# Optimization experiments

Measured on AMD Instinct MI355X. Metric: run time of the kernel, lower is better.

## Reference

```python
import jax, jax.numpy as jnp
import numpy as np

VOCAB = 50257
WINDOW = 2048
EMB = 256
BATCH = 8


def setup_inputs() -> dict:
    key = jax.random.key(0)
    ks = jax.random.split(key, 9)
    s = 0.02
    x = jax.random.randint(ks[0], (BATCH, WINDOW), 0, VOCAB, dtype=jnp.int64 if jax.config.jax_enable_x64 else jnp.int32)
    tok_emb = jax.random.normal(ks[1], (VOCAB, EMB), dtype=jnp.float32) * s
    pos_emb = jax.random.normal(ks[2], (WINDOW, EMB), dtype=jnp.float32) * s
    Wq = jax.random.normal(ks[3], (EMB, EMB), dtype=jnp.float32) * s
    bq = jnp.zeros((EMB,), dtype=jnp.float32)
    Wk = jax.random.normal(ks[4], (EMB, EMB), dtype=jnp.float32) * s
    bk = jnp.zeros((EMB,), dtype=jnp.float32)
    Wv = jax.random.normal(ks[5], (EMB, EMB), dtype=jnp.float32) * s
    bv = jnp.zeros((EMB,), dtype=jnp.float32)
    return {"x": x, "tok_emb": tok_emb, "pos_emb": pos_emb,
            "Wq": Wq, "bq": bq, "Wk": Wk, "bk": bk, "Wv": Wv, "bv": bv}


def reference(x, tok_emb, pos_emb, Wq, bq, Wk, bk, Wv, bv):
    # h: [B, T, E] = token embedding + full-window position embedding
    h = tok_emb[x] + pos_emb[None, :, :]
    q = jnp.einsum('bte,fe->btf', h, Wq) + bq
    k = jnp.einsum('bte,fe->btf', h, Wk) + bk
    v = jnp.einsum('bte,fe->btf', h, Wv) + bv
    # NOTE: original module has NO 1/sqrt(d) scaling -- keep faithful.
    scores = jnp.einsum('bqe,bke->bqk', q, k)  # [B, T, T]
    T = scores.shape[-1]
    causal = jnp.tril(jnp.ones((T, T), dtype=bool))
    scores = jnp.where(causal[None, :, :], scores, -jnp.inf)
    weight = jax.nn.softmax(scores, axis=-1)
    attention_output = jnp.einsum('bqk,bke->bqe', weight, v)  # [B, T, E]
    return attention_output
```

## Files before the change

### kernel.cpp

```cpp
#include <hip/hip_runtime.h>


#define TWIN 2048
#define NEMB 256
#define NB   8
#define VOCAB 50257
#define NTOK (NB * TWIN)

typedef __attribute__((ext_vector_type(8))) short s16x8;
typedef __attribute__((ext_vector_type(4))) float f32x4;
typedef __attribute__((ext_vector_type(4))) float f4;
typedef unsigned short u16;
typedef unsigned int   u32;

__device__ __forceinline__ u16 f2bf(float f) {
    union { float f; u32 i; } x; x.f = f;
    u32 r = x.i + 0x7fffu + ((x.i >> 16) & 1u);
    return (u16)(r >> 16);
}
__device__ __forceinline__ float bf2f(u16 u) {
    union { u32 i; float f; } x; x.i = ((u32)u) << 16; return x.f;
}
__device__ __forceinline__ u32 pack2bf(float a, float b) {
    return (u32)f2bf(a) | ((u32)f2bf(b) << 16);
}
__device__ __forceinline__ void gload_lds16(const void* g, void* l) {
    __builtin_amdgcn_global_load_lds(
        (const __attribute__((address_space(1))) void*)g,
        (__attribute__((address_space(3))) void*)l, 16, 0, 0);
}

__global__ __launch_bounds__(256) void wconv_kernel(
    const float* __restrict__ Wq, const float* __restrict__ Wk,
    const float* __restrict__ Wv, u16* __restrict__ Wb)
{
    int b = blockIdx.x;
    int which = b >> 5;
    int off = (b & 31) * 2048 + threadIdx.x * 8;
    const float* src = (which == 0) ? Wq : ((which == 1) ? Wk : Wv);
    f4 v0 = *(const f4*)(src + off);
    f4 v1 = *(const f4*)(src + off + 4);
    u16 ww[8];
#pragma unroll
    for (int i = 0; i < 4; i++) { ww[i] = f2bf(v0[i]); ww[4 + i] = f2bf(v1[i]); }
    *(uint4*)(Wb + which * 65536 + off) = *(uint4*)ww;
}

__global__ __launch_bounds__(256) void tok_prep(const void* xraw, int* tokidx) {
    const long long* x64 = (const long long*)xraw;
    const int*       x32 = (const int*)xraw;
    long long probe = x64[threadIdx.x & 63];
    int ok = (probe >= 0 && probe < VOCAB) ? 1 : 0;
    int is64 = __all(ok);
    int i = blockIdx.x * 256 + threadIdx.x;
    int v = is64 ? (int)x64[i] : x32[i];
    tokidx[i] = (v < 0) ? 0 : ((v >= VOCAB) ? (VOCAB - 1) : v);
}

__global__ __launch_bounds__(128) void qkv_kernel(
    const int* __restrict__ tokidx,
    const float* __restrict__ tok, const float* __restrict__ pos,
    const u16* __restrict__ Wb,
    const float* __restrict__ bqp, const float* __restrict__ bkp,
    const float* __restrict__ bvp,
    u16* __restrict__ Qg, u16* __restrict__ Kg, u16* __restrict__ Vt)
{
    __shared__ u16 h_lds[32 * 256];

    const int tid   = threadIdx.x;
    const int which = blockIdx.x >> 9;
    const int t0    = (blockIdx.x & 511) * 32;
    const int bb    = t0 >> 11;
    const int tl0   = t0 & (TWIN - 1);

#pragma unroll
    for (int j = 0; j < 8; j++) {
        int c   = tid + 128 * j;
        int row = c >> 5, col = c & 31;
        int t   = t0 + row;
        int xi  = tokidx[t];
        const float* tp = tok + (size_t)xi * NEMB + col * 8;
        const float* pp = pos + (size_t)(t & (TWIN - 1)) * NEMB + col * 8;
        f4 a0 = *(const f4*)tp, a1 = *(const f4*)(tp + 4);
        f4 b0 = *(const f4*)pp, b1 = *(const f4*)(pp + 4);
        u16 hh[8];
#pragma unroll
        for (int i = 0; i < 4; i++) {
            hh[i]     = f2bf(a0[i] + b0[i]);
            hh[4 + i] = f2bf(a1[i] + b1[i]);
        }
        *(uint4*)((char*)h_lds + row * 512 + ((col * 16) ^ ((row & 7) << 4))) = *(uint4*)hh;
    }
    __syncthreads();

    const int wid = tid >> 6, lane = tid & 63, g = lane >> 4, lr = lane & 15;
    const u16* Wp = Wb + which * 65536;
    const float* Bp = (which == 0) ? bqp : ((which == 1) ? bkp : bvp);

    f32x4 acc[16];
#pragma unroll
    for (int i = 0; i < 16; i++) acc[i] = (f32x4){0.f, 0.f, 0.f, 0.f};

#pragma unroll
    for (int es = 0; es < 8; es++) {
        int arow = wid * 16 + lr;
        s16x8 af = *(const s16x8*)((const char*)h_lds + arow * 512 +
                                   ((es * 64 + g * 16) ^ ((arow & 7) << 4)));
        s16x8 bfv[16];
#pragma unroll
        for (int ct = 0; ct < 16; ct++)
            bfv[ct] = *(const s16x8*)(Wp + (size_t)(ct * 16 + lr) * NEMB + es * 32 + g * 8);
#pragma unroll
        for (int ct = 0; ct < 16; ct++)
            acc[ct] = __builtin_amdgcn_mfma_f32_16x16x32_bf16(af, bfv[ct], acc[ct], 0, 0, 0);
    }

    if (which < 2) {
        u16* dst = (which == 0) ? Qg : Kg;
        __syncthreads();
#pragma unroll
        for (int ct = 0; ct < 16; ct++) {
            float bias = Bp[ct * 16 + lr];
#pragma unroll
            for (int r = 0; r < 4; r++)
                h_lds[(wid * 16 + 4 * g + r) * 256 + ct * 16 + lr] = f2bf(acc[ct][r] + bias);
        }
        __syncthreads();
#pragma unroll
        for (int j = 0; j < 8; j++) {
            int c = tid + 128 * j;
            int row = c >> 5, col = c & 31;
            uint4 v = *(const uint4*)(h_lds + row * 256 + col * 8);
            *(uint4*)(dst + (size_t)(t0 + row) * NEMB + col * 8) = v;
        }
    } else {
#pragma unroll
        for (int ct = 0; ct < 16; ct++) {
            float bias = Bp[ct * 16 + lr];
            u16 pk[4];
#pragma unroll
            for (int r = 0; r < 4; r++) pk[r] = f2bf(acc[ct][r] + bias);
            int e = ct * 16 + lr;
            *(ushort4*)(Vt + ((size_t)bb * NEMB + e) * TWIN + tl0 + wid * 16 + 4 * g)
                = *(ushort4*)pk;
        }
    }
}

__global__ __launch_bounds__(256) void attn_partial(
    const u16* __restrict__ Qg, const u16* __restrict__ Kg,
    const u16* __restrict__ Vt, u16* __restrict__ Ppart,
    float* __restrict__ Pm, float* __restrict__ Pl)
{
    __shared__ char smem[65536];

    const int bid = blockIdx.x;
    const int bb  = bid & 7;
    const int idx = bid >> 3;
    int J, cc;
    if (idx < 17)      { J = 31 - idx; cc = 0; }
    else if (idx < 33) { J = 48 - idx; cc = 1; }
    else               { J = 47 - idx; cc = 0; }
    const int ntJ = 2 * J + 2;
    const int ts  = cc * 32;
    const int te  = (ntJ < ts + 32) ? ntJ : (ts + 32);
    const int n   = te - ts;
    const int cid = bb * 48 + ((cc == 0) ? J : (32 + J - 16));

    const u16* Qb = Qg + (size_t)bb * TWIN * NEMB;
    const u16* Kb = Kg + (size_t)bb * TWIN * NEMB;
    const u16* Vb = Vt + (size_t)bb * NEMB * TWIN;

    const int tid = threadIdx.x;
    const int w = tid >> 6, lane = tid & 63;
    const int q = lane & 15, hi = lane >> 4;
    const int qrow = J * 64 + w * 16 + q;

    s16x8 qf[8];
#pragma unroll
    for (int es = 0; es < 8; es++)
        qf[es] = *(const s16x8*)(Qb + (size_t)qrow * NEMB + es * 32 + hi * 8);

    #define STAGE(buf_, kb_)                                                          \
    {                                                                                 \
        char* base = smem + (buf_) * 32768;                                           \
        const int kbq_ = (kb_);                                                       \
        if (w < 2) {                                                                  \
            _Pragma("unroll")                                                         \
            for (int i2 = 0; i2 < 8; i2++) {                                          \
                int gc = w * 8 + i2;                                                  \
                int s = gc * 64 + lane;                                               \
                int row = s >> 5, col16 = s & 31;                                     \
                const char* src = (const char*)(Kb + (size_t)(kbq_ + row) * NEMB)     \
                                  + ((col16 * 16) ^ ((row & 7) << 4));                \
                gload_lds16(src, base + gc * 1024);                                   \
            }                                                                         \
        } else {                                                                      \
            _Pragma("unroll")                                                         \
            for (int i2 = 0; i2 < 8; i2++) {                                          \
                int gv = (w - 2) * 8 + i2;                                            \
                int s = gv * 64 + lane;                                               \
                int rr = s >> 8, ee = s & 255;                                        \
                const char* src = (const char*)(Vb + (size_t)ee * TWIN + kbq_ + rr * 8); \
                gload_lds16(src, base + 16384 + gv * 1024);                           \
            }                                                                         \
        }                                                                             \
    }

    STAGE(0, ts * 32)
    if (n > 1) STAGE(1, (ts + 1) * 32)

    f32x4 o[16];
#pragma unroll
    for (int i = 0; i < 16; i++) o[i] = (f32x4){0.f, 0.f, 0.f, 0.f};
    float m = -1.0e4f, l = 0.f;

    for (int t = 0; t < n; t++) {
        const int kb = (ts + t) * 32;
        const char* kbase = smem + (t & 1) * 32768;
        const char* vbase = kbase + 16384;

        if (t + 1 < n) asm volatile("s_waitcnt vmcnt(8)" ::: "memory");
        else           asm volatile("s_waitcnt vmcnt(0)" ::: "memory");
        asm volatile("s_barrier" ::: "memory");

        f32x4 st0 = (f32x4){0.f, 0.f, 0.f, 0.f};
        f32x4 st1 = (f32x4){0.f, 0.f, 0.f, 0.f};
#pragma unroll
        for (int es = 0; es < 8; es++) {
            s16x8 kf0 = *(const s16x8*)(kbase + q * 512 +
                                        ((es * 64 + hi * 16) ^ ((q & 7) << 4)));
            st0 = __builtin_amdgcn_mfma_f32_16x16x32_bf16(kf0, qf[es], st0, 0, 0, 0);
            int row1 = q + 16;
            s16x8 kf1 = *(const s16x8*)(kbase + row1 * 512 +
                                        ((es * 64 + hi * 16) ^ ((row1 & 7) << 4)));
            st1 = __builtin_amdgcn_mfma_f32_16x16x32_bf16(kf1, qf[es], st1, 0, 0, 0);
        }

        if (kb + 31 > qrow) {
#pragma unroll
            for (int r = 0; r < 4; r++) {
                if (kb + 4 * hi + r > qrow)      st0[r] = -1.0e4f;
                if (kb + 16 + 4 * hi + r > qrow) st1[r] = -1.0e4f;
            }
        }

        float tm = fmaxf(fmaxf(fmaxf(st0[0], st0[1]), fmaxf(st0[2], st0[3])),
                         fmaxf(fmaxf(st1[0], st1[1]), fmaxf(st1[2], st1[3])));
        tm = fmaxf(tm, __shfl_xor(tm, 16));
        tm = fmaxf(tm, __shfl_xor(tm, 32));
        if (__any(tm > m)) {
            float mn = fmaxf(m, tm);
            float sc = __expf(m - mn);
            m = mn; l *= sc;
            float scr[4];
#pragma unroll
            for (int r = 0; r < 4; r++) scr[r] = __shfl(sc, hi * 20 + r);
#pragma unroll
            for (int et = 0; et < 16; et++)
#pragma unroll
                for (int r = 0; r < 4; r++) o[et][r] *= scr[r];
        }
        float p0[4], p1[4];
#pragma unroll
        for (int r = 0; r < 4; r++) {
            p0[r] = __expf(st0[r] - m);
            p1[r] = __expf(st1[r] - m);
        }
        float rs = (p0[0] + p0[1]) + (p0[2] + p0[3]) + (p1[0] + p1[1]) + (p1[2] + p1[3]);
        rs += __shfl_xor(rs, 16);
        rs += __shfl_xor(rs, 32);
        l += rs;

        u32 pk00 = pack2bf(p0[0], p0[1]), pk01 = pack2bf(p0[2], p0[3]);
        u32 pk10 = pack2bf(p1[0], p1[1]), pk11 = pack2bf(p1[2], p1[3]);
        int sA = (lane & 15) | ((lane & 16) << 1);
        int sB = sA + 16;
        u32 b00 = (u32)__shfl((int)pk00, sA), b01 = (u32)__shfl((int)pk01, sA);
        u32 b02 = (u32)__shfl((int)pk00, sB), b03 = (u32)__shfl((int)pk01, sB);
        u32 b10 = (u32)__shfl((int)pk10, sA), b11 = (u32)__shfl((int)pk11, sA);
        u32 b12 = (u32)__shfl((int)pk10, sB), b13 = (u32)__shfl((int)pk11, sB);
        bool c1 = (hi & 2) != 0;
        union { uint4 u; s16x8 v; } pu;
        pu.u.x = c1 ? b10 : b00;
        pu.u.y = c1 ? b11 : b01;
        pu.u.z = c1 ? b12 : b02;
        pu.u.w = c1 ? b13 : b03;
        s16x8 pf = pu.v;

#pragma unroll
        for (int et = 0; et < 16; et++) {
            s16x8 vf = *(const s16x8*)(vbase + hi * 4096 + (q + 16 * et) * 16);
            o[et] = __builtin_amdgcn_mfma_f32_16x16x32_bf16(pf, vf, o[et], 0, 0, 0);
        }

        asm volatile("s_barrier" ::: "memory");
        if (t + 2 < n) STAGE((t & 1), (ts + t + 2) * 32)
    }
    #undef STAGE

    if (hi == 0) {
        Pm[cid * 64 + w * 16 + q] = m;
        Pl[cid * 64 + w * 16 + q] = l;
    }
    u16* Pp = Ppart + (size_t)cid * 16384;
#pragma unroll
    for (int et = 0; et < 16; et++)
#pragma unroll
        for (int r = 0; r < 4; r++)
            Pp[(w * 16 + 4 * hi + r) * 256 + q + 16 * et] = f2bf(o[et][r]);
}

__global__ __launch_bounds__(256) void attn_combine(
    const u16* __restrict__ Ppart, const float* __restrict__ Pm,
    const float* __restrict__ Pl, float* __restrict__ outp)
{
    const int bid = blockIdx.x;
    const int bb  = bid & 7;
    const int qt  = bid >> 3;
    const int tid = threadIdx.x;
    const int r   = tid >> 3;
    const int cg  = tid & 7;
    const int J   = qt >> 1;
    const int rr  = (qt & 1) * 32 + r;

    const int cidA = bb * 48 + J;
    const float mA = Pm[cidA * 64 + rr], lA = Pl[cidA * 64 + rr];
    const u16* pA = Ppart + (size_t)cidA * 16384 + rr * 256 + cg * 32;

    float wa, wb;
    const u16* pB = nullptr;
    if (J >= 16) {
        const int cidB = bb * 48 + 32 + (J - 16);
        float mB = Pm[cidB * 64 + rr], lB = Pl[cidB * 64 + rr];
        pB = Ppart + (size_t)cidB * 16384 + rr * 256 + cg * 32;
        float M = fmaxf(mA, mB);
        wa = __expf(mA - M); wb = __expf(mB - M);
        float inv = 1.0f / (lA * wa + lB * wb);
        wa *= inv; wb *= inv;
    } else {
        wa = 1.0f / lA; wb = 0.f;
    }

    float* dst = outp + ((size_t)bb * TWIN + qt * 32 + r) * NEMB + cg * 32;
#pragma unroll
    for (int v4 = 0; v4 < 4; v4++) {
        uint4 a = *(const uint4*)(pA + v4 * 8);
        u32 au[4] = {a.x, a.y, a.z, a.w};
        float ov[8];
#pragma unroll
        for (int i = 0; i < 4; i++) {
            ov[2 * i]     = bf2f((u16)(au[i] & 0xffffu)) * wa;
            ov[2 * i + 1] = bf2f((u16)(au[i] >> 16)) * wa;
        }
        if (pB) {
            uint4 b = *(const uint4*)(pB + v4 * 8);
            u32 bu[4] = {b.x, b.y, b.z, b.w};
#pragma unroll
            for (int i = 0; i < 4; i++) {
                ov[2 * i]     += bf2f((u16)(bu[i] & 0xffffu)) * wb;
                ov[2 * i + 1] += bf2f((u16)(bu[i] >> 16)) * wb;
            }
        }
#pragma unroll
        for (int i = 0; i < 8; i++) dst[v4 * 8 + i] = ov[i];
    }
}

__global__ __launch_bounds__(256) void ws_diag(float* outp, int n, float val) {
    int i = blockIdx.x * 256 + threadIdx.x;
    if (i < n) outp[i] = (i == 0) ? val : 0.0f;
}

extern "C" void kernel_launch(void* const* d_in, const int* in_sizes, int n_in,
                              void* d_out, int out_size, void* d_ws, size_t ws_size,
                              hipStream_t stream)
{
    const void*  x   = d_in[0];
    const float* tok = (const float*)d_in[1];
    const float* pos = (const float*)d_in[2];
    const float* Wq  = (const float*)d_in[3];
    const float* bq  = (const float*)d_in[4];
    const float* Wk  = (const float*)d_in[5];
    const float* bk  = (const float*)d_in[6];
    const float* Wv  = (const float*)d_in[7];
    const float* bv  = (const float*)d_in[8];

    const size_t kvElems  = (size_t)NB * TWIN * NEMB;
    const size_t wbElems  = 3 * 65536;
    const size_t nChunks  = 48 * NB;
    const size_t pmBytes  = nChunks * 64 * sizeof(float);
    const size_t ppBytes  = nChunks * 16384 * sizeof(u16);

    const size_t needSplit = 2 * kvElems * 2 + wbElems * 2 + NTOK * 4
                           + 2 * pmBytes + ppBytes + 256;

    if (ws_size < needSplit) {
        float val = 1000.0f + (float)(ws_size >> 20);
        hipLaunchKernelGGL(ws_diag, dim3((out_size + 255) / 256), dim3(256), 0, stream,
                           (float*)d_out, out_size, val);
        return;
    }

    u16* Kg = (u16*)d_ws;
    u16* Vt = Kg + kvElems;
    u16* Wb = Vt + kvElems;
    int* tokidx = (int*)(Wb + wbElems);
    float* Pm = (float*)((char*)tokidx + NTOK * 4);
    float* Pl = (float*)((char*)Pm + pmBytes);
    u16* Ppart = (u16*)((char*)Pl + pmBytes);
    u16* Qg = (u16*)d_out;

    hipLaunchKernelGGL(wconv_kernel, dim3(96), dim3(256), 0, stream, Wq, Wk, Wv, Wb);
    hipLaunchKernelGGL(tok_prep, dim3(64), dim3(256), 0, stream, x, tokidx);
    hipLaunchKernelGGL(qkv_kernel, dim3(1536), dim3(128), 0, stream,
                       tokidx, tok, pos, Wb, bq, bk, bv, Qg, Kg, Vt);
    hipLaunchKernelGGL(attn_partial, dim3(384), dim3(256), 0, stream,
                       Qg, Kg, Vt, Ppart, Pm, Pl);
    hipLaunchKernelGGL(attn_combine, dim3(512), dim3(256), 0, stream,
                       Ppart, Pm, Pl, (float*)d_out);
}
```

Baseline: 157.0 us.

## Software-pipeline QK of next tile with softmax and load V directly to registers

Restructures the attention inner loop so the QK^T MFMAs for the next key tile are issued before the softmax of the current tile, overlapping MFMA with the exp/shuffle work. V fragments are now loaded straight from global memory into registers with inline asm instead of being staged through LDS. The LDS buffer shrinks to hold only K tiles, and each wave loads a quarter of K. This cuts LDS footprint and traffic, which may allow more resident blocks, but it raises register pressure (16 uint4 V fragments plus two score sets) and relies on hand-written vmcnt counts that must match the load order exactly.

New measurement: 169.7 us. 8.1% more time.

```diff
diff --git a/kernel.cpp b/kernel.cpp
--- a/kernel.cpp
+++ b/kernel.cpp
@@ -152,7 +152,7 @@
     const u16* __restrict__ Vt, u16* __restrict__ Ppart,
     float* __restrict__ Pm, float* __restrict__ Pl)
 {
-    __shared__ char smem[65536];
+    __shared__ char smem[32768];
 
     const int bid = blockIdx.x;
     const int bb  = bid & 7;
@@ -181,123 +181,172 @@
     for (int es = 0; es < 8; es++)
         qf[es] = *(const s16x8*)(Qb + (size_t)qrow * NEMB + es * 32 + hi * 8);
 
-    #define STAGE(buf_, kb_)                                                          \
+    #define KSTAGE(buf_, kb_)                                                         \
     {                                                                                 \
-        char* base = smem + (buf_) * 32768;                                           \
+        char* base = smem + (buf_) * 16384;                                           \
         const int kbq_ = (kb_);                                                       \
-        if (w < 2) {                                                                  \
+        _Pragma("unroll")                                                             \
+        for (int i2 = 0; i2 < 4; i2++) {                                              \
+            int gc = w * 4 + i2;                                                      \
+            int s = gc * 64 + lane;                                                   \
+            int row = s >> 5, col16 = s & 31;                                         \
+            const char* src = (const char*)(Kb + (size_t)(kbq_ + row) * NEMB)         \
+                              + ((col16 * 16) ^ ((row & 7) << 4));                    \
+            gload_lds16(src, base + gc * 1024);                                       \
+        }                                                                             \
+    }
+
+    #define QKCOMP(st0_, st1_, buf_, kb_)                                             \
+    {                                                                                 \
+        const char* kp = smem + (buf_) * 16384;                                       \
+        const int kb2_ = (kb_);                                                       \
+        _Pragma("unroll")                                                             \
+        for (int es = 0; es < 8; es++) {                                              \
+            s16x8 kf0 = *(const s16x8*)(kp + q * 512 +                                \
+                                        ((es * 64 + hi * 16) ^ ((q & 7) << 4)));      \
+            st0_ = __builtin_amdgcn_mfma_f32_16x16x32_bf16(kf0, qf[es], st0_, 0,0,0); \
+            int row1 = q + 16;                                                        \
+            s16x8 kf1 = *(const s16x8*)(kp + row1 * 512 +                             \
+                                        ((es * 64 + hi * 16) ^ ((row1 & 7) << 4)));   \
+            st1_ = __builtin_amdgcn_mfma_f32_16x16x32_bf16(kf1, qf[es], st1_, 0,0,0); \
+        }                                                                             \
+        if (kb2_ + 31 > qrow) {                                                       \
             _Pragma("unroll")                                                         \
-            for (int i2 = 0; i2 < 8; i2++) {                                          \
-                int gc = w * 8 + i2;                                                  \
-                int s = gc * 64 + lane;                                               \
-                int row = s >> 5, col16 = s & 31;                                     \
-                const char* src = (const char*)(Kb + (size_t)(kbq_ + row) * NEMB)     \
-                                  + ((col16 * 16) ^ ((row & 7) << 4));                \
-                gload_lds16(src, base + gc * 1024);                                   \
-            }                                                                         \
-        } else {                                                                      \
-            _Pragma("unroll")                                                         \
-            for (int i2 = 0; i2 < 8; i2++) {                                          \
-                int gv = (w - 2) * 8 + i2;                                            \
-                int s = gv * 64 + lane;                                               \
-                int rr = s >> 8, ee = s & 255;                                        \
-                const char* src = (const char*)(Vb + (size_t)ee * TWIN + kbq_ + rr * 8); \
-                gload_lds16(src, base + 16384 + gv * 1024);                           \
+            for (int r = 0; r < 4; r++) {                                             \
+                if (kb2_ + 4 * hi + r > qrow)      st0_[r] = -1.0e4f;                 \
+                if (kb2_ + 16 + 4 * hi + r > qrow) st1_[r] = -1.0e4f;                 \
             }                                                                         \
         }                                                                             \
     }
 
-    STAGE(0, ts * 32)
-    if (n > 1) STAGE(1, (ts + 1) * 32)
+    #define SOFTMAX_RELAYOUT(st0_, st1_, pf_)                                         \
+    {                                                                                 \
+        float tm = fmaxf(fmaxf(fmaxf(st0_[0], st0_[1]), fmaxf(st0_[2], st0_[3])),     \
+                         fmaxf(fmaxf(st1_[0], st1_[1]), fmaxf(st1_[2], st1_[3])));    \
+        tm = fmaxf(tm, __shfl_xor(tm, 16));                                           \
+        tm = fmaxf(tm, __shfl_xor(tm, 32));                                           \
+        if (__any(tm > m)) {                                                          \
+            float mn = fmaxf(m, tm);                                                  \
+            float sc = __expf(m - mn);                                                \
+            m = mn; l *= sc;                                                          \
+            float scr[4];                                                             \
+            _Pragma("unroll")                                                         \
+            for (int r = 0; r < 4; r++) scr[r] = __shfl(sc, hi * 20 + r);             \
+            _Pragma("unroll")                                                         \
+            for (int et = 0; et < 16; et++)                                           \
+                _Pragma("unroll")                                                     \
+                for (int r = 0; r < 4; r++) o[et][r] *= scr[r];                       \
+        }                                                                             \
+        float p0[4], p1[4];                                                           \
+        _Pragma("unroll")                                                             \
+        for (int r = 0; r < 4; r++) {                                                 \
+            p0[r] = __expf(st0_[r] - m);                                              \
+            p1[r] = __expf(st1_[r] - m);                                              \
+        }                                                                             \
+        float rs = (p0[0]+p0[1])+(p0[2]+p0[3])+(p1[0]+p1[1])+(p1[2]+p1[3]);           \
+        rs += __shfl_xor(rs, 16);                                                     \
+        rs += __shfl_xor(rs, 32);                                                     \
+        l += rs;                                                                      \
+        u32 pk00 = pack2bf(p0[0], p0[1]), pk01 = pack2bf(p0[2], p0[3]);               \
+        u32 pk10 = pack2bf(p1[0], p1[1]), pk11 = pack2bf(p1[2], p1[3]);               \
+        int sA = (lane & 15) | ((lane & 16) << 1);                                    \
+        int sB = sA + 16;                                                             \
+        u32 b00 = (u32)__shfl((int)pk00, sA), b01 = (u32)__shfl((int)pk01, sA);       \
+        u32 b02 = (u32)__shfl((int)pk00, sB), b03 = (u32)__shfl((int)pk01, sB);       \
+        u32 b10 = (u32)__shfl((int)pk10, sA), b11 = (u32)__shfl((int)pk11, sA);       \
+        u32 b12 = (u32)__shfl((int)pk10, sB), b13 = (u32)__shfl((int)pk11, sB);       \
+        bool c1 = (hi & 2) != 0;                                                      \
+        union { uint4 u; s16x8 v; } pu;                                               \
+        pu.u.x = c1 ? b10 : b00;                                                      \
+        pu.u.y = c1 ? b11 : b01;                                                      \
+        pu.u.z = c1 ? b12 : b02;                                                      \
+        pu.u.w = c1 ? b13 : b03;                                                      \
+        pf_ = pu.v;                                                                   \
+    }
 
     f32x4 o[16];
 #pragma unroll
     for (int i = 0; i < 16; i++) o[i] = (f32x4){0.f, 0.f, 0.f, 0.f};
     float m = -1.0e4f, l = 0.f;
 
-    for (int t = 0; t < n; t++) {
+    KSTAGE(0, ts * 32)
+    if (n > 1) {
+        KSTAGE(1, (ts + 1) * 32)
+        asm volatile("s_waitcnt vmcnt(4)" ::: "memory");
+    } else {
+        asm volatile("s_waitcnt vmcnt(0)" ::: "memory");
+    }
+    __builtin_amdgcn_sched_barrier(0);
+    asm volatile("s_barrier" ::: "memory");
+
+    f32x4 stA0 = (f32x4){0.f, 0.f, 0.f, 0.f};
+    f32x4 stA1 = (f32x4){0.f, 0.f, 0.f, 0.f};
+    QKCOMP(stA0, stA1, 0, ts * 32)
+
+    for (int t = 0; t < n - 1; t++) {
         const int kb = (ts + t) * 32;
-        const char* kbase = smem + (t & 1) * 32768;
-        const char* vbase = kbase + 16384;
-
-        if (t + 1 < n) asm volatile("s_waitcnt vmcnt(8)" ::: "memory");
+
+        uint4 vf[16];
+        {
+            unsigned long long va =
+                (unsigned long long)(Vb + (size_t)q * TWIN + kb + hi * 8);
+#pragma unroll
+            for (int et = 0; et < 16; et++) {
+                asm volatile("global_load_dwordx4 %0, %1, off"
+                             : "=&v"(vf[et]) : "v"(va) : "memory");
+                va += (unsigned long long)16 * TWIN * 2;
+            }
+        }
+        asm volatile("s_waitcnt vmcnt(16)" ::: "memory");
+        __builtin_amdgcn_sched_barrier(0);
+        asm volatile("s_barrier" ::: "memory");
+        if (t + 2 < n) KSTAGE((t & 1), (ts + t + 2) * 32)
+
+        f32x4 stB0 = (f32x4){0.f, 0.f, 0.f, 0.f};
+        f32x4 stB1 = (f32x4){0.f, 0.f, 0.f, 0.f};
+        QKCOMP(stB0, stB1, ((t + 1) & 1), kb + 32)
+        s16x8 pf;
+        SOFTMAX_RELAYOUT(stA0, stA1, pf)
+
+        if (t + 2 < n) asm volatile("s_waitcnt vmcnt(4)" ::: "memory");
         else           asm volatile("s_waitcnt vmcnt(0)" ::: "memory");
-        asm volatile("s_barrier" ::: "memory");
-
-        f32x4 st0 = (f32x4){0.f, 0.f, 0.f, 0.f};
-        f32x4 st1 = (f32x4){0.f, 0.f, 0.f, 0.f};
-#pragma unroll
-        for (int es = 0; es < 8; es++) {
-            s16x8 kf0 = *(const s16x8*)(kbase + q * 512 +
-                                        ((es * 64 + hi * 16) ^ ((q & 7) << 4)));
-            st0 = __builtin_amdgcn_mfma_f32_16x16x32_bf16(kf0, qf[es], st0, 0, 0, 0);
-            int row1 = q + 16;
-            s16x8 kf1 = *(const s16x8*)(kbase + row1 * 512 +
-                                        ((es * 64 + hi * 16) ^ ((row1 & 7) << 4)));
-            st1 = __builtin_amdgcn_mfma_f32_16x16x32_bf16(kf1, qf[es], st1, 0, 0, 0);
-        }
-
-        if (kb + 31 > qrow) {
-#pragma unroll
-            for (int r = 0; r < 4; r++) {
-                if (kb + 4 * hi + r > qrow)      st0[r] = -1.0e4f;
-                if (kb + 16 + 4 * hi + r > qrow) st1[r] = -1.0e4f;
+        __builtin_amdgcn_sched_barrier(0);
+
+#pragma unroll
+        for (int et = 0; et < 16; et++) {
+            union { uint4 u; s16x8 v; } vu; vu.u = vf[et];
+            o[et] = __builtin_amdgcn_mfma_f32_16x16x32_bf16(pf, vu.v, o[et], 0, 0, 0);
+        }
+
+        stA0 = stB0; stA1 = stB1;
+    }
+
+    {
+        const int kb = (ts + n - 1) * 32;
+        uint4 vf[16];
+        {
+            unsigned long long va =
+                (unsigned long long)(Vb + (size_t)q * TWIN + kb + hi * 8);
+#pragma unroll
+            for (int et = 0; et < 16; et++) {
+                asm volatile("global_load_dwordx4 %0, %1, off"
+                             : "=&v"(vf[et]) : "v"(va) : "memory");
+                va += (unsigned long long)16 * TWIN * 2;
             }
         }
-
-        float tm = fmaxf(fmaxf(fmaxf(st0[0], st0[1]), fmaxf(st0[2], st0[3])),
-                         fmaxf(fmaxf(st1[0], st1[1]), fmaxf(st1[2], st1[3])));
-        tm = fmaxf(tm, __shfl_xor(tm, 16));
-        tm = fmaxf(tm, __shfl_xor(tm, 32));
-        if (__any(tm > m)) {
-            float mn = fmaxf(m, tm);
-            float sc = __expf(m - mn);
-            m = mn; l *= sc;
-            float scr[4];
-#pragma unroll
-            for (int r = 0; r < 4; r++) scr[r] = __shfl(sc, hi * 20 + r);
-#pragma unroll
-            for (int et = 0; et < 16; et++)
-#pragma unroll
-                for (int r = 0; r < 4; r++) o[et][r] *= scr[r];
-        }
-        float p0[4], p1[4];
-#pragma unroll
-        for (int r = 0; r < 4; r++) {
-            p0[r] = __expf(st0[r] - m);
-            p1[r] = __expf(st1[r] - m);
-        }
-        float rs = (p0[0] + p0[1]) + (p0[2] + p0[3]) + (p1[0] + p1[1]) + (p1[2] + p1[3]);
-        rs += __shfl_xor(rs, 16);
-        rs += __shfl_xor(rs, 32);
-        l += rs;
-
-        u32 pk00 = pack2bf(p0[0], p0[1]), pk01 = pack2bf(p0[2], p0[3]);
-        u32 pk10 = pack2bf(p1[0], p1[1]), pk11 = pack2bf(p1[2], p1[3]);
-        int sA = (lane & 15) | ((lane & 16) << 1);
-        int sB = sA + 16;
-        u32 b00 = (u32)__shfl((int)pk00, sA), b01 = (u32)__shfl((int)pk01, sA);
-        u32 b02 = (u32)__shfl((int)pk00, sB), b03 = (u32)__shfl((int)pk01, sB);
-        u32 b10 = (u32)__shfl((int)pk10, sA), b11 = (u32)__shfl((int)pk11, sA);
-        u32 b12 = (u32)__shfl((int)pk10, sB), b13 = (u32)__shfl((int)pk11, sB);
-        bool c1 = (hi & 2) != 0;
-        union { uint4 u; s16x8 v; } pu;
-        pu.u.x = c1 ? b10 : b00;
-        pu.u.y = c1 ? b11 : b01;
-        pu.u.z = c1 ? b12 : b02;
-        pu.u.w = c1 ? b13 : b03;
-        s16x8 pf = pu.v;
-
+        s16x8 pf;
+        SOFTMAX_RELAYOUT(stA0, stA1, pf)
+        asm volatile("s_waitcnt vmcnt(0)" ::: "memory");
+        __builtin_amdgcn_sched_barrier(0);
 #pragma unroll
         for (int et = 0; et < 16; et++) {
-            s16x8 vf = *(const s16x8*)(vbase + hi * 4096 + (q + 16 * et) * 16);
-            o[et] = __builtin_amdgcn_mfma_f32_16x16x32_bf16(pf, vf, o[et], 0, 0, 0);
-        }
-
-        asm volatile("s_barrier" ::: "memory");
-        if (t + 2 < n) STAGE((t & 1), (ts + t + 2) * 32)
-    }
-    #undef STAGE
+            union { uint4 u; s16x8 v; } vu; vu.u = vf[et];
+            o[et] = __builtin_amdgcn_mfma_f32_16x16x32_bf16(pf, vu.v, o[et], 0, 0, 0);
+        }
+    }
+    #undef KSTAGE
+    #undef QKCOMP
+    #undef SOFTMAX_RELAYOUT
 
     if (hi == 0) {
         Pm[cid * 64 + w * 16 + q] = m;
```
